# Performance work log

Hardware: AMD Instinct MI355X
Metric: run time of the kernel (lower is better)

The kernel has to match this reference:

```python
import jax, jax.numpy as jnp
import numpy as np

# Model dims (from dispatcher config)
V, H, L, I, KD = 32000, 1024, 3, 4096, 256
NH, NKV, HD = 16, 4, 64          # head_dim = H/NH = KD/NKV = 64
G = NH // NKV                     # heads per KV group = 4
B, S = 2, 1024
BLOCK, NSUB = 512, 5              # process_output: first 5 subblocks of 512 rows
TOPL = 3                          # 'deep' focus -> top-3 layers


def setup_inputs() -> dict:
    key = jax.random.key(0)
    ks = jax.random.split(key, 16)
    w = lambda k, shape: jax.random.normal(k, shape, jnp.float32) * 0.02
    return {
        "input_ids": jax.random.randint(ks[0], (B, S), 0, V),
        "emb": w(ks[1], (V, H)),              # embedding_layer
        "shortcut_emb": w(ks[2], (1000, H)),  # shortcut_embed
        "Wq": w(ks[3], (L, H, H)),            # per-layer q_proj blocks (single block0 each)
        "Wk": w(ks[4], (L, KD, H)),
        "Wv": w(ks[5], (L, KD, H)),
        "Wo": w(ks[6], (L, H, H)),
        "Wgate": w(ks[7], (L, I, H)),
        "Wup": w(ks[8], (L, I, H)),
        "Wdown": w(ks[9], (L, H, I)),
        "Wls": w(ks[10], (L, H)),             # layer_scorer
        "bls": jnp.zeros((L,), jnp.float32),
        "Wbs": w(ks[11], (1, H)),             # block_scorer
        "bbs": jnp.zeros((1,), jnp.float32),
        "Wout": w(ks[12], (4096, H)),         # output weight block (split into 512-row subblocks)
    }


def _forward(input_ids, emb, shortcut_emb, Wq, Wk, Wv, Wo,
             Wgate, Wup, Wdown, Wls, bls, Wbs, bbs, Wout):
    b, s = input_ids.shape
    # is_common: all ids < 1000 -> shortcut embedding (prev_context None on fresh call)
    is_common = jnp.all(input_ids < 1000)
    h = jnp.where(is_common,
                  shortcut_emb[jnp.clip(input_ids, 0, 999)],
                  emb[input_ids])                       # [B,S,H]

    # select_layers ('deep' focus): top-3 layers by layer_scorer on batch elem 0
    layer_scores = h.mean(axis=1)[0] @ Wls.T + bls      # [L]
    _, sel = jax.lax.top_k(layer_scores, TOPL)

    for i in range(TOPL):
        li = sel[i]                                     # dynamic layer gather
        wq, wk, wv, wo = Wq[li], Wk[li], Wv[li], Wo[li]
        wg, wu, wd = Wgate[li], Wup[li], Wdown[li]

        # scan_layer: quick q projection -> block_scorer sigmoid gate
        quick_q = h @ wq.T                              # [B,S,H]
        gate = jax.nn.sigmoid(quick_q.mean(axis=1) @ Wbs.T + bbs) > 0.5  # [B,1]

        # process_attention: manual GQA with threshold-masked softmax
        q = (h @ wq.T).reshape(b, s, NKV, G, HD).transpose(0, 2, 3, 1, 4)  # [B,KV,G,S,D]
        k = (h @ wk.T).reshape(b, s, NKV, HD).transpose(0, 2, 1, 3)        # [B,KV,S,D]
        v = (h @ wv.T).reshape(b, s, NKV, HD).transpose(0, 2, 1, 3)        # [B,KV,S,D]
        scores = jnp.einsum('bhgsd,bhqd->bhgsq', q, k) / (HD ** 0.5)       # [B,KV,G,S,S]
        aw = jax.nn.softmax(scores, axis=-1)
        aw = aw * (aw > 0.01)                           # hard threshold mask
        v_exp = jnp.broadcast_to(v[:, :, None], (b, NKV, G, s, HD))
        # NOTE: faithful to source einsum 'bhgsq,bhgsd->bhgsd': sums aw over q and scales v
        attn = jnp.einsum('bhgsq,bhgsd->bhgsd', aw, v_exp)
        attn = attn.transpose(0, 3, 1, 2, 4).reshape(b, s, H)
        attn = attn @ wo.T

        # process_mlp: gate*up (no activation in source), then down
        new_h = ((attn @ wg.T) * (attn @ wu.T)) @ wd.T

        h = jnp.where(gate[:, :, None], new_h, h)       # scan_layer gate per batch elem

    # process_output: concat first 5 subblocks of 512 rows, matmul with transpose
    combined = Wout[:BLOCK * NSUB]                      # [2560, H]
    return h @ combined.T                               # [B,S,2560]


def reference(input_ids, emb, shortcut_emb, Wq, Wk, Wv, Wo,
              Wgate, Wup, Wdown, Wls, bls, Wbs, bbs, Wout):
    return _forward(input_ids, emb, shortcut_emb, Wq, Wk, Wv, Wo,
                    Wgate, Wup, Wdown, Wls, bls, Wbs, bbs, Wout)
```

## Files before the change

kernel.cpp:

```cpp
#include <hip/hip_runtime.h>
#include <hip/hip_bf16.h>

constexpr int kH = 1024, kS = 1024, kNH = 16, kI = 4096, kNOUT = 2560;
constexpr int kQKVN = 1536;

typedef __attribute__((ext_vector_type(8))) short short8v;
typedef __attribute__((ext_vector_type(4))) float f32x4;
typedef unsigned short u16;

#define MFMA16 __builtin_amdgcn_mfma_f32_16x16x32_bf16

__device__ __forceinline__ u16 f2bf(float f) {
  unsigned u = __float_as_uint(f);
  return (u16)((u + 0x7fffu + ((u >> 16) & 1u)) >> 16);
}
__device__ __forceinline__ float bf2f(u16 u) {
  return __uint_as_float(((unsigned)u) << 16);
}
__device__ __forceinline__ unsigned cvt2bf(float lo, float hi) {
  unsigned r;
  asm("v_cvt_pk_bf16_f32 %0, %1, %2" : "=v"(r) : "v"(lo), "v"(hi));
  return r;
}
__device__ __forceinline__ void gload16(void* lds, const void* g) {
  __builtin_amdgcn_global_load_lds(
      (const __attribute__((address_space(1))) unsigned int*)g,
      (__attribute__((address_space(3))) unsigned int*)lds, 16, 0, 0);
}

constexpr long OFF_H    = 0;
constexpr long OFF_HMP  = OFF_H + 2097152;
constexpr long OFF_INT  = OFF_HMP + 16384;
constexpr long OFF_GV   = OFF_INT + 64;
constexpr long OFF_HBF  = OFF_GV + 3072;
constexpr long OFF_QKV  = OFF_HBF + 1048576;
constexpr long OFF_ATT  = OFF_QKV + 1572864;
constexpr long OFF_OBF  = OFF_ATT + 1048576;
constexpr long OFF_PBF  = OFF_OBF + 1048576;

__global__ void embed_gv_kernel(const int* __restrict__ ids, const float* __restrict__ emb,
                                const float* __restrict__ semb, const float* __restrict__ Wq,
                                const float* __restrict__ Wbs, float* __restrict__ h,
                                u16* __restrict__ hbf, float* __restrict__ gv,
                                int* __restrict__ ip) {
  int bid = blockIdx.x, tid = threadIdx.x;
  if (bid < 2048) {
    __shared__ int oks;
    if (tid == 0) oks = 1;
    __syncthreads();
    int ok = 1;
    for (int i = tid; i < 2048; i += 256) ok &= (ids[i] < 1000) ? 1 : 0;
    if (!ok) atomicAnd(&oks, 0);
    __syncthreads();
    int common = oks;
    long row = bid;
    int id = ids[row];
    int cid = id < 0 ? 0 : (id > 999 ? 999 : id);
    const float4* s4 = (const float4*)(common ? semb + (long)cid * kH : emb + (long)id * kH);
    float4 v = s4[tid];
    *((float4*)(h + row * kH) + tid) = v;
    ushort4 u;
    u.x = f2bf(v.x); u.y = f2bf(v.y); u.z = f2bf(v.z); u.w = f2bf(v.w);
    *((ushort4*)(hbf + row * kH) + tid) = u;
  } else if (bid < 2240) {
    int q = bid - 2048;
    int l = q >> 6, j0 = (q & 63) * 16;
    int jj = tid & 15, cg = tid >> 4;
    const float* wq = Wq + (long)l * 1048576;
    float acc = 0.f;
    for (int c = cg * 64; c < cg * 64 + 64; ++c)
      acc += Wbs[c] * wq[(long)c * kH + j0 + jj];
    __shared__ float red[256];
    red[tid] = acc;
    __syncthreads();
    if (tid < 16) {
      float s = 0.f;
      #pragma unroll
      for (int g = 0; g < 16; ++g) s += red[g * 16 + tid];
      gv[l * 1024 + j0 + tid] = s;
    }
  } else {
    if (tid < 32) ip[tid] = 0;
  }
}

template <int FIRST>
__global__ __launch_bounds__(256) void hmean_fused_kernel(
    const float* __restrict__ h, float* __restrict__ hmp, const float* __restrict__ gv,
    const float* __restrict__ Wls, const float* __restrict__ bls,
    const float* __restrict__ bbs, int* __restrict__ ip, int layer_i,
    int* __restrict__ cnt) {
  int tid = threadIdx.x;
  int c = blockIdx.x * 256 + tid, b = blockIdx.y, z = blockIdx.z;
  float a = 0.f;
  if (!ip[16 + b]) {
    const float* p = h + ((long)b << 20) + ((long)z << 17) + c;
    #pragma unroll 4
    for (int r = 0; r < 128; ++r) a += p[(long)r << 10];
  }
  hmp[z * 2048 + b * 1024 + c] = a;
  __threadfence();
  __syncthreads();
  __shared__ int lastf;
  if (tid == 0) lastf = (atomicAdd(cnt, 1) == 63) ? 1 : 0;
  __syncthreads();
  if (!lastf) return;
  __threadfence();

  float hm0[4], hm1[4];
  #pragma unroll
  for (int u = 0; u < 4; ++u) {
    int j = tid + u * 256;
    float s0 = 0.f, s1 = 0.f;
    #pragma unroll
    for (int z2 = 0; z2 < 8; ++z2) {
      s0 += hmp[z2 * 2048 + j];
      s1 += hmp[z2 * 2048 + 1024 + j];
    }
    hm0[u] = s0; hm1[u] = s1;
  }
  __shared__ float red[3][256];
  __shared__ int sli;
  int li;
  if constexpr (FIRST) {
    float a0 = 0.f, a1 = 0.f, a2 = 0.f;
    #pragma unroll
    for (int u = 0; u < 4; ++u) {
      int j = tid + u * 256;
      a0 += hm0[u] * Wls[j];
      a1 += hm0[u] * Wls[kH + j];
      a2 += hm0[u] * Wls[2 * kH + j];
    }
    red[0][tid] = a0; red[1][tid] = a1; red[2][tid] = a2;
    __syncthreads();
    for (int st = 128; st; st >>= 1) {
      if (tid < st) {
        red[0][tid] += red[0][tid + st];
        red[1][tid] += red[1][tid + st];
        red[2][tid] += red[2][tid + st];
      }
      __syncthreads();
    }
    if (tid == 0) {
      float sc[3] = {red[0][0] * (1.f / kS) + bls[0], red[1][0] * (1.f / kS) + bls[1],
                     red[2][0] * (1.f / kS) + bls[2]};
      int aa = 0;
      if (sc[1] > sc[aa]) aa = 1;
      if (sc[2] > sc[aa]) aa = 2;
      int b2 = -1; float bb = -3.4e38f;
      for (int i = 0; i < 3; ++i)
        if (i != aa && sc[i] > bb) { bb = sc[i]; b2 = i; }
      ip[1] = aa; ip[2] = b2; ip[3] = 3 - aa - b2;
      sli = aa;
    }
    __syncthreads();
    li = sli;
  } else {
    li = ip[1 + layer_i];
  }
  float g0 = 0.f, g1 = 0.f;
  #pragma unroll
  for (int u = 0; u < 4; ++u) {
    int j = tid + u * 256;
    float v = gv[li * 1024 + j];
    g0 += v * hm0[u];
    g1 += v * hm1[u];
  }
  __syncthreads();
  red[0][tid] = g0; red[1][tid] = g1;
  __syncthreads();
  for (int st = 128; st; st >>= 1) {
    if (tid < st) { red[0][tid] += red[0][tid + st]; red[1][tid] += red[1][tid + st]; }
    __syncthreads();
  }
  if (tid == 0) {
    int* g = ip + 4 + 2 * layer_i;
    g[0] = ((red[0][0] * (1.f / kS) + bbs[0]) > 0.f) ? 1 : 0;
    g[1] = ((red[1][0] * (1.f / kS) + bbs[0]) > 0.f) ? 1 : 0;
  }
}

template <int MODE>
__global__ __launch_bounds__(256) void gemm_bf_kernel(
    const u16* __restrict__ A, const float* __restrict__ Bf0, const float* __restrict__ Bf1,
    const float* __restrict__ Bf2, void* __restrict__ C0,
    int N, int K, const int* __restrict__ li_p,
    const int* __restrict__ gate, const int* __restrict__ hz) {
  __shared__ u16 As[128 * 64];
  __shared__ u16 Bs[64 * 64];

  const int m0 = blockIdx.y * 128, n0 = blockIdx.x * 64;
  const int tid = threadIdx.x;
  const int bb = m0 >> 10;

  if (MODE == 4 && hz != nullptr && hz[bb]) {
    int r = tid >> 1, cb = n0 + (tid & 1) * 32;
    float* c0 = (float*)C0 + (long)(m0 + r) * N + cb;
    float4 z4 = make_float4(0.f, 0.f, 0.f, 0.f);
    #pragma unroll
    for (int j = 0; j < 32; j += 4) *(float4*)(c0 + j) = z4;
    return;
  }
  if (MODE == 0) {
    if (!gate[bb]) return;
    if (hz != nullptr && hz[bb]) return;
  }

  long li = (MODE == 4) ? 0 : (long)(*li_p);
  const float* bsrc;
  if constexpr (MODE == 0) {
    if (n0 < 1024)      bsrc = Bf0 + li * 1048576 + (long)n0 * kH;
    else if (n0 < 1280) bsrc = Bf1 + li * 262144 + (long)(n0 - 1024) * kH;
    else                bsrc = Bf2 + li * 262144 + (long)(n0 - 1280) * kH;
  } else {
    bsrc = Bf0 + (long)n0 * kH;
  }

  const int wave = tid >> 6, lane = tid & 63;
  const int lr = lane & 15, lg = lane >> 4;
  const int wm = wave >> 1, wn = wave & 1;

  f32x4 acc[4][2] = {};

  const int sr = tid >> 3, sc8 = tid & 7;
  const int sr1 = (tid + 256) >> 3;

  for (int k0 = 0; k0 < K; k0 += 64) {
    #pragma unroll
    for (int j = 0; j < 4; ++j) {
      int c = tid + j * 256;
      int r = c >> 3, c8 = c & 7;
      gload16((char*)As + (wave * 64 + j * 256) * 16,
              A + (long)(m0 + r) * K + k0 + ((c8 ^ (r & 7)) * 8));
    }
    #pragma unroll
    for (int j = 0; j < 2; ++j) {
      int r = j ? sr1 : sr, c8 = sc8;
      const float* p = bsrc + (long)r * K + k0 + c8 * 8;
      float4 v0 = *(const float4*)p;
      float4 v1 = *(const float4*)(p + 4);
      union { short8v s8; unsigned u[4]; } uo;
      uo.u[0] = cvt2bf(v0.x, v0.y);
      uo.u[1] = cvt2bf(v0.z, v0.w);
      uo.u[2] = cvt2bf(v1.x, v1.y);
      uo.u[3] = cvt2bf(v1.z, v1.w);
      *(short8v*)((char*)Bs + ((r * 128 + c8 * 16) ^ ((r & 7) << 4))) = uo.s8;
    }
    __syncthreads();
    #pragma unroll
    for (int kh = 0; kh < 2; ++kh) {
      const int kb = kh * 64 + lg * 16;
      short8v av[4], bv[2];
      #pragma unroll
      for (int mi = 0; mi < 4; ++mi) {
        int r = wm * 64 + mi * 16 + lr;
        av[mi] = *(const short8v*)((const char*)As + ((r * 128 + kb) ^ ((r & 7) << 4)));
      }
      #pragma unroll
      for (int ni = 0; ni < 2; ++ni) {
        int r = wn * 32 + ni * 16 + lr;
        bv[ni] = *(const short8v*)((const char*)Bs + ((r * 128 + kb) ^ ((r & 7) << 4)));
      }
      #pragma unroll
      for (int mi = 0; mi < 4; ++mi)
        #pragma unroll
        for (int ni = 0; ni < 2; ++ni)
          acc[mi][ni] = MFMA16(av[mi], bv[ni], acc[mi][ni], 0, 0, 0);
    }
    __syncthreads();
  }
  #pragma unroll
  for (int mi = 0; mi < 4; ++mi)
    #pragma unroll
    for (int ni = 0; ni < 2; ++ni)
      #pragma unroll
      for (int r = 0; r < 4; ++r) {
        long idx = (long)(m0 + wm * 64 + mi * 16 + lg * 4 + r) * N +
                   (n0 + wn * 32 + ni * 16 + lr);
        float v = acc[mi][ni][r];
        if constexpr (MODE == 0) ((u16*)C0)[idx] = f2bf(v);
        else ((float*)C0)[idx] = v;
      }
}

__device__ __forceinline__ void dev_barrier(int* cnt, int target) {
  __syncthreads();
  __threadfence();
  if (threadIdx.x == 0) {
    atomicAdd(cnt, 1);
    while (atomicAdd(cnt, 0) < target) __builtin_amdgcn_s_sleep(8);
  }
  __syncthreads();
  __threadfence();
}

template <int PH>
__device__ __forceinline__ void mlp_tile(int t, long li, const u16* __restrict__ A,
                                         const float* __restrict__ B0base,
                                         const float* __restrict__ B1base,
                                         void* __restrict__ C0, void* __restrict__ C1,
                                         int ac0, int ac1, u16* As, u16* Bs, u16* Bs1) {
  constexpr bool USE_B1 = (PH == 1);
  constexpr int N = (PH == 1) ? 4096 : 1024;
  constexpr int K = (PH == 2) ? 4096 : 1024;
  const int tid = threadIdx.x;
  const int tm = t & 15, tn = t >> 4;
  const int m0 = tm * 128, n0 = tn * 64;
  if (!((tm >> 3) ? ac1 : ac0)) return;

  const float* bsrc;
  const float* bsrc1 = nullptr;
  if constexpr (PH == 0) {
    bsrc = B0base + li * 1048576 + (long)n0 * 1024;
  } else if constexpr (PH == 1) {
    bsrc = B0base + li * 4194304 + (long)n0 * 1024;
    bsrc1 = B1base + li * 4194304 + (long)n0 * 1024;
  } else {
    bsrc = B0base + li * 4194304 + (long)n0 * 4096;
  }

  const int wave = tid >> 6, lane = tid & 63;
  const int lr = lane & 15, lg = lane >> 4;
  const int wm = wave >> 1, wn = wave & 1;

  f32x4 acc[4][2] = {};
  f32x4 acc1[USE_B1 ? 4 : 1][2] = {};

  const int sr = tid >> 3, sc8 = tid & 7;
  const int sr1 = (tid + 256) >> 3;

  for (int k0 = 0; k0 < K; k0 += 64) {
    #pragma unroll
    for (int j = 0; j < 4; ++j) {
      int c = tid + j * 256;
      int r = c >> 3, c8 = c & 7;
      gload16((char*)As + (wave * 64 + j * 256) * 16,
              A + (long)(m0 + r) * K + k0 + ((c8 ^ (r & 7)) * 8));
    }
    #pragma unroll
    for (int j = 0; j < 2; ++j) {
      int r = j ? sr1 : sr, c8 = sc8;
      const float* p = bsrc + (long)r * K + k0 + c8 * 8;
      float4 v0 = *(const float4*)p;
      float4 v1 = *(const float4*)(p + 4);
      union { short8v s8; unsigned u[4]; } uo;
      uo.u[0] = cvt2bf(v0.x, v0.y);
      uo.u[1] = cvt2bf(v0.z, v0.w);
      uo.u[2] = cvt2bf(v1.x, v1.y);
      uo.u[3] = cvt2bf(v1.z, v1.w);
      *(short8v*)((char*)Bs + ((r * 128 + c8 * 16) ^ ((r & 7) << 4))) = uo.s8;
      if constexpr (USE_B1) {
        const float* p1 = bsrc1 + (long)r * K + k0 + c8 * 8;
        float4 w0 = *(const float4*)p1;
        float4 w1 = *(const float4*)(p1 + 4);
        union { short8v s8; unsigned u[4]; } uo1;
        uo1.u[0] = cvt2bf(w0.x, w0.y);
        uo1.u[1] = cvt2bf(w0.z, w0.w);
        uo1.u[2] = cvt2bf(w1.x, w1.y);
        uo1.u[3] = cvt2bf(w1.z, w1.w);
        *(short8v*)((char*)Bs1 + ((r * 128 + c8 * 16) ^ ((r & 7) << 4))) = uo1.s8;
      }
    }
    __syncthreads();
    #pragma unroll
    for (int kh = 0; kh < 2; ++kh) {
      const int kb = kh * 64 + lg * 16;
      short8v av[4], bv[2], b1v[2];
      #pragma unroll
      for (int mi = 0; mi < 4; ++mi) {
        int r = wm * 64 + mi * 16 + lr;
        av[mi] = *(const short8v*)((const char*)As + ((r * 128 + kb) ^ ((r & 7) << 4)));
      }
      #pragma unroll
      for (int ni = 0; ni < 2; ++ni) {
        int r = wn * 32 + ni * 16 + lr;
        int byte = (r * 128 + kb) ^ ((r & 7) << 4);
        bv[ni] = *(const short8v*)((const char*)Bs + byte);
        if constexpr (USE_B1) b1v[ni] = *(const short8v*)((const char*)Bs1 + byte);
      }
      #pragma unroll
      for (int mi = 0; mi < 4; ++mi)
        #pragma unroll
        for (int ni = 0; ni < 2; ++ni) {
          acc[mi][ni] = MFMA16(av[mi], bv[ni], acc[mi][ni], 0, 0, 0);
          if constexpr (USE_B1)
            acc1[mi][ni] = MFMA16(av[mi], b1v[ni], acc1[mi][ni], 0, 0, 0);
        }
    }
    __syncthreads();
  }
  #pragma unroll
  for (int mi = 0; mi < 4; ++mi)
    #pragma unroll
    for (int ni = 0; ni < 2; ++ni)
      #pragma unroll
      for (int r = 0; r < 4; ++r) {
        long idx = (long)(m0 + wm * 64 + mi * 16 + lg * 4 + r) * N +
                   (n0 + wn * 32 + ni * 16 + lr);
        float v = acc[mi][ni][r];
        if constexpr (PH == 0) ((u16*)C0)[idx] = f2bf(v);
        if constexpr (PH == 1) ((u16*)C0)[idx] = f2bf(v * acc1[mi][ni][r]);
        if constexpr (PH == 2) { ((float*)C0)[idx] = v; ((u16*)C1)[idx] = f2bf(v); }
      }
}

__global__ __launch_bounds__(256) void mlp_kernel(
    const u16* __restrict__ ATT, const float* __restrict__ Wo, const float* __restrict__ Wg,
    const float* __restrict__ Wu, const float* __restrict__ Wd, u16* __restrict__ Obf,
    u16* __restrict__ Pbf, float* __restrict__ h, u16* __restrict__ hbf,
    const int* __restrict__ li_p, const int* __restrict__ gate,
    const int* __restrict__ act, int* __restrict__ hzwr, int* __restrict__ cnt2) {
  const int tid = threadIdx.x, bid = blockIdx.x;
  int g0 = gate[0], g1 = gate[1];
  int a0 = act[0], a1 = act[1];
  if (bid == 0 && tid == 0) {
    if (g0) hzwr[0] = a0 ? 0 : 1;
    if (g1) hzwr[1] = a1 ? 0 : 1;
  }
  int ac0 = g0 && a0, ac1 = g1 && a1;
  if (!ac0 && !ac1) return;

  __shared__ u16 As[128 * 64];
  __shared__ u16 Bs[64 * 64];
  __shared__ u16 Bs1[64 * 64];
  long li = (long)(*li_p);

  mlp_tile<0>(bid, li, ATT, Wo, nullptr, Obf, nullptr, ac0, ac1, As, Bs, Bs1);
  dev_barrier(cnt2 + 0, 256);
  for (int t = bid; t < 1024; t += 256)
    mlp_tile<1>(t, li, Obf, Wg, Wu, Pbf, nullptr, ac0, ac1, As, Bs, Bs1);
  dev_barrier(cnt2 + 1, 256);
  mlp_tile<2>(bid, li, Pbf, Wd, nullptr, h, hbf, ac0, ac1, As, Bs, Bs1);
}

__global__ __launch_bounds__(256) void rowsum_kernel(
    const u16* __restrict__ QKV, const int* __restrict__ gate, int* __restrict__ act,
    const int* __restrict__ hz, u16* __restrict__ ATT) {
  int b = blockIdx.z;
  if (!gate[b] || hz[b]) return;
  int kvg = blockIdx.y, qt = blockIdx.x;
  int tid = threadIdx.x;
  int w = tid >> 6, lane = tid & 63, lr = lane & 15, lg = lane >> 4;

  __shared__ float sm[4][64], ss[4][64], st[4][64], srs[64];
  __shared__ int sflags;
  if (tid == 0) sflags = 0;

  long qrow = ((long)b << 10) + qt * 16 + lr;
  short8v qlo[4], qhi[4];
  #pragma unroll
  for (int hh = 0; hh < 4; ++hh) {
    const u16* qp = QKV + qrow * kQKVN + (kvg * 4 + hh) * 64 + lg * 8;
    qlo[hh] = *(const short8v*)qp;
    qhi[hh] = *(const short8v*)(qp + 32);
  }
  const u16* kb0 = QKV + (((long)b << 10) + w * 256 + lr) * kQKVN + 1024 + kvg * 64 + lg * 8;

  float s[4][4], pm[4][4];
  #pragma unroll
  for (int hh = 0; hh < 4; ++hh)
    #pragma unroll
    for (int i = 0; i < 4; ++i) { s[hh][i] = 0.f; pm[hh][i] = -3e38f; }
  for (int kt = 0; kt < 16; ++kt) {
    const u16* kp = kb0 + (long)kt * 16 * kQKVN;
    short8v klo = *(const short8v*)kp;
    short8v khi = *(const short8v*)(kp + 32);
    #pragma unroll
    for (int hh = 0; hh < 4; ++hh) {
      f32x4 c = {0.f, 0.f, 0.f, 0.f};
      c = MFMA16(qlo[hh], klo, c, 0, 0, 0);
      c = MFMA16(qhi[hh], khi, c, 0, 0, 0);
      #pragma unroll
      for (int i = 0; i < 4; ++i) {
        float x = c[i] * 0.125f;
        s[hh][i] += __expf(x);
        pm[hh][i] = fmaxf(pm[hh][i], x);
      }
    }
  }
  #pragma unroll
  for (int off = 1; off < 16; off <<= 1)
    #pragma unroll
    for (int hh = 0; hh < 4; ++hh)
      #pragma unroll
      for (int i = 0; i < 4; ++i) {
        s[hh][i] += __shfl_xor(s[hh][i], off);
        pm[hh][i] = fmaxf(pm[hh][i], __shfl_xor(pm[hh][i], off));
      }
  if (lr == 0)
    #pragma unroll
    for (int hh = 0; hh < 4; ++hh)
      #pragma unroll
      for (int i = 0; i < 4; ++i) {
        sm[w][hh * 16 + lg * 4 + i] = pm[hh][i];
        ss[w][hh * 16 + lg * 4 + i] = s[hh][i];
      }
  __syncthreads();
  float Mg[4][4], Sg[4][4];
  int myfl = 0;
  #pragma unroll
  for (int hh = 0; hh < 4; ++hh)
    #pragma unroll
    for (int i = 0; i < 4; ++i) {
      int q = hh * 16 + lg * 4 + i;
      float mm = fmaxf(fmaxf(sm[0][q], sm[1][q]), fmaxf(sm[2][q], sm[3][q]));
      float SS = ss[0][q] + ss[1][q] + ss[2][q] + ss[3][q];
      Mg[hh][i] = mm; Sg[hh][i] = SS;
      if (mm > 60.f) myfl |= 2;
      if (__expf(mm) > 0.01f * SS) myfl |= 1;
    }
  if (myfl) atomicOr(&sflags, myfl);
  __syncthreads();
  int flags = sflags;

  if (flags & 2) {
    #pragma unroll
    for (int hh = 0; hh < 4; ++hh)
      #pragma unroll
      for (int i = 0; i < 4; ++i) s[hh][i] = 0.f;
    for (int kt = 0; kt < 16; ++kt) {
      const u16* kp = kb0 + (long)kt * 16 * kQKVN;
      short8v klo = *(const short8v*)kp;
      short8v khi = *(const short8v*)(kp + 32);
      #pragma unroll
      for (int hh = 0; hh < 4; ++hh) {
        f32x4 c = {0.f, 0.f, 0.f, 0.f};
        c = MFMA16(qlo[hh], klo, c, 0, 0, 0);
        c = MFMA16(qhi[hh], khi, c, 0, 0, 0);
        #pragma unroll
        for (int i = 0; i < 4; ++i) s[hh][i] += __expf(c[i] * 0.125f - Mg[hh][i]);
      }
    }
    #pragma unroll
    for (int off = 1; off < 16; off <<= 1)
      #pragma unroll
      for (int hh = 0; hh < 4; ++hh)
        #pragma unroll
        for (int i = 0; i < 4; ++i) s[hh][i] += __shfl_xor(s[hh][i], off);
    if (lr == 0)
      #pragma unroll
      for (int hh = 0; hh < 4; ++hh)
        #pragma unroll
        for (int i = 0; i < 4; ++i) ss[w][hh * 16 + lg * 4 + i] = s[hh][i];
    __syncthreads();
    #pragma unroll
    for (int hh = 0; hh < 4; ++hh)
      #pragma unroll
      for (int i = 0; i < 4; ++i) {
        int q = hh * 16 + lg * 4 + i;
        Sg[hh][i] = ss[0][q] + ss[1][q] + ss[2][q] + ss[3][q];
      }
    __syncthreads();
  }
  float shift = (flags & 2) ? 1.f : 0.f;

  if (flags & 1) {
    float tt[4][4] = {};
    for (int kt = 0; kt < 16; ++kt) {
      const u16* kp = kb0 + (long)kt * 16 * kQKVN;
      short8v klo = *(const short8v*)kp;
      short8v khi = *(const short8v*)(kp + 32);
      #pragma unroll
      for (int hh = 0; hh < 4; ++hh) {
        f32x4 c = {0.f, 0.f, 0.f, 0.f};
        c = MFMA16(qlo[hh], klo, c, 0, 0, 0);
        c = MFMA16(qhi[hh], khi, c, 0, 0, 0);
        #pragma unroll
        for (int i = 0; i < 4; ++i) {
          float e = __expf(c[i] * 0.125f - shift * Mg[hh][i]);
          if (e > 0.01f * Sg[hh][i]) tt[hh][i] += e;
        }
      }
    }
    #pragma unroll
    for (int off = 1; off < 16; off <<= 1)
      #pragma unroll
      for (int hh = 0; hh < 4; ++hh)
        #pragma unroll
        for (int i = 0; i < 4; ++i) tt[hh][i] += __shfl_xor(tt[hh][i], off);
    if (lr == 0)
      #pragma unroll
      for (int hh = 0; hh < 4; ++hh)
        #pragma unroll
        for (int i = 0; i < 4; ++i) st[w][hh * 16 + lg * 4 + i] = tt[hh][i];
  }
  __syncthreads();
  if (tid < 64) {
    int hh = tid >> 4, q = tid & 15;
    int qq = hh * 16 + q;
    float T = (flags & 1) ? (st[0][qq] + st[1][qq] + st[2][qq] + st[3][qq]) : 0.f;
    float SS = ss[0][qq] + ss[1][qq] + ss[2][qq] + ss[3][qq];
    srs[qq] = T / SS;
    if (T > 0.f) atomicOr(act + b, 1);
  }
  __syncthreads();
  int hh = tid >> 6, rr = (tid >> 2) & 15, d0 = (tid & 3) * 16;
  float rv = srs[hh * 16 + rr];
  long row = ((long)b << 10) + qt * 16 + rr;
  const u16* vp = QKV + row * kQKVN + 1280 + kvg * 64 + d0;
  u16* op = ATT + row * kH + (kvg * 4 + hh) * 64 + d0;
  #pragma unroll
  for (int j = 0; j < 16; j += 4) {
    ushort4 v = *(const ushort4*)(vp + j);
    ushort4 o;
    o.x = f2bf(rv * bf2f(v.x)); o.y = f2bf(rv * bf2f(v.y));
    o.z = f2bf(rv * bf2f(v.z)); o.w = f2bf(rv * bf2f(v.w));
    *(ushort4*)(op + j) = o;
  }
}

extern "C" void kernel_launch(void* const* d_in, const int* in_sizes, int n_in,
                              void* d_out, int out_size, void* d_ws, size_t ws_size,
                              hipStream_t stream) {
  (void)in_sizes; (void)n_in; (void)out_size; (void)ws_size;
  const int*   ids  = (const int*)d_in[0];
  const float* emb  = (const float*)d_in[1];
  const float* semb = (const float*)d_in[2];
  const float* Wq   = (const float*)d_in[3];
  const float* Wk   = (const float*)d_in[4];
  const float* Wv   = (const float*)d_in[5];
  const float* Wo   = (const float*)d_in[6];
  const float* Wg   = (const float*)d_in[7];
  const float* Wu   = (const float*)d_in[8];
  const float* Wd   = (const float*)d_in[9];
  const float* Wls  = (const float*)d_in[10];
  const float* bls  = (const float*)d_in[11];
  const float* Wbs  = (const float*)d_in[12];
  const float* bbs  = (const float*)d_in[13];
  const float* Wout = (const float*)d_in[14];
  float* out = (float*)d_out;
  float* ws  = (float*)d_ws;

  float* h   = ws + OFF_H;
  float* hmp = ws + OFF_HMP;
  int* ip    = (int*)(ws + OFF_INT);
  int* sel   = ip + 1;
  int* gate  = ip + 4;
  int* act   = ip + 10;
  int* hzb   = ip + 16;
  int* cnt   = ip + 20;
  int* bar   = ip + 24;
  float* gv  = ws + OFF_GV;
  u16* hbf   = (u16*)(ws + OFF_HBF);
  u16* QKV   = (u16*)(ws + OFF_QKV);
  u16* ATT   = (u16*)(ws + OFF_ATT);
  u16* Obf   = (u16*)(ws + OFF_OBF);
  u16* Pbf   = (u16*)(ws + OFF_PBF);

  embed_gv_kernel<<<2241, 256, 0, stream>>>(ids, emb, semb, Wq, Wbs, h, hbf, gv, ip);

  for (int i = 0; i < 3; i++) {
    const int* li = sel + i;
    int* g_i = gate + 2 * i;
    int* a_i = act + 2 * i;

    if (i == 0)
      hmean_fused_kernel<1><<<dim3(4, 2, 8), 256, 0, stream>>>(h, hmp, gv, Wls, bls, bbs,
                                                               ip, 0, cnt + 0);
    else
      hmean_fused_kernel<0><<<dim3(4, 2, 8), 256, 0, stream>>>(h, hmp, gv, Wls, bls, bbs,
                                                               ip, i, cnt + i);
    gemm_bf_kernel<0><<<dim3(kQKVN / 64, 16), 256, 0, stream>>>(
        hbf, Wq, Wk, Wv, QKV, kQKVN, kH, li, g_i, hzb);
    rowsum_kernel<<<dim3(64, 4, 2), 256, 0, stream>>>(QKV, g_i, a_i, hzb, ATT);
    mlp_kernel<<<256, 256, 0, stream>>>(ATT, Wo, Wg, Wu, Wd, Obf, Pbf, h, hbf,
                                        li, g_i, a_i, hzb, bar + 2 * i);
  }
  gemm_bf_kernel<4><<<dim3(kNOUT / 64, 16), 256, 0, stream>>>(
      hbf, Wout, nullptr, nullptr, out, kNOUT, kH, nullptr, nullptr, hzb);
}
```

Before: 137.3 us.

## Fuse per-layer kernels into one persistent kernel with device-wide barriers

Replaces the four kernel launches per layer (hmean, QKV gemm, rowsum, mlp) and the final output gemm with one persistent 384-block kernel per layer. Phases are separated by a software grid barrier, and the output projection is folded into the last layer's kernel. The aim is to remove launch gaps and idle tails between the small dependent stages. In exchange it adds spin-wait barriers and requires all 384 blocks to be co-resident (launch bounds 2 per CU), or the kernel deadlocks. The barrier counters live in the ip area, which the embed kernel now zeroes more of.

```diff
diff --git a/kernel.cpp b/kernel.cpp
--- a/kernel.cpp
+++ b/kernel.cpp
@@ -3,6 +3,7 @@
 
 constexpr int kH = 1024, kS = 1024, kNH = 16, kI = 4096, kNOUT = 2560;
 constexpr int kQKVN = 1536;
+constexpr int GRID = 384;
 
 typedef __attribute__((ext_vector_type(8))) short short8v;
 typedef __attribute__((ext_vector_type(4))) float f32x4;
@@ -26,6 +27,17 @@
   __builtin_amdgcn_global_load_lds(
       (const __attribute__((address_space(1))) unsigned int*)g,
       (__attribute__((address_space(3))) unsigned int*)lds, 16, 0, 0);
+}
+
+__device__ __forceinline__ void dev_barrier(int* cnt, int target) {
+  __syncthreads();
+  __threadfence();
+  if (threadIdx.x == 0) {
+    atomicAdd(cnt, 1);
+    while (atomicAdd(cnt, 0) < target) __builtin_amdgcn_s_sleep(8);
+  }
+  __syncthreads();
+  __threadfence();
 }
 
 constexpr long OFF_H    = 0;
@@ -80,163 +92,44 @@
       gv[l * 1024 + j0 + tid] = s;
     }
   } else {
-    if (tid < 32) ip[tid] = 0;
-  }
-}
-
-template <int FIRST>
-__global__ __launch_bounds__(256) void hmean_fused_kernel(
-    const float* __restrict__ h, float* __restrict__ hmp, const float* __restrict__ gv,
-    const float* __restrict__ Wls, const float* __restrict__ bls,
-    const float* __restrict__ bbs, int* __restrict__ ip, int layer_i,
-    int* __restrict__ cnt) {
-  int tid = threadIdx.x;
-  int c = blockIdx.x * 256 + tid, b = blockIdx.y, z = blockIdx.z;
-  float a = 0.f;
-  if (!ip[16 + b]) {
-    const float* p = h + ((long)b << 20) + ((long)z << 17) + c;
-    #pragma unroll 4
-    for (int r = 0; r < 128; ++r) a += p[(long)r << 10];
-  }
-  hmp[z * 2048 + b * 1024 + c] = a;
-  __threadfence();
-  __syncthreads();
-  __shared__ int lastf;
-  if (tid == 0) lastf = (atomicAdd(cnt, 1) == 63) ? 1 : 0;
-  __syncthreads();
-  if (!lastf) return;
-  __threadfence();
-
-  float hm0[4], hm1[4];
-  #pragma unroll
-  for (int u = 0; u < 4; ++u) {
-    int j = tid + u * 256;
-    float s0 = 0.f, s1 = 0.f;
-    #pragma unroll
-    for (int z2 = 0; z2 < 8; ++z2) {
-      s0 += hmp[z2 * 2048 + j];
-      s1 += hmp[z2 * 2048 + 1024 + j];
-    }
-    hm0[u] = s0; hm1[u] = s1;
-  }
-  __shared__ float red[3][256];
-  __shared__ int sli;
-  int li;
-  if constexpr (FIRST) {
-    float a0 = 0.f, a1 = 0.f, a2 = 0.f;
-    #pragma unroll
-    for (int u = 0; u < 4; ++u) {
-      int j = tid + u * 256;
-      a0 += hm0[u] * Wls[j];
-      a1 += hm0[u] * Wls[kH + j];
-      a2 += hm0[u] * Wls[2 * kH + j];
-    }
-    red[0][tid] = a0; red[1][tid] = a1; red[2][tid] = a2;
-    __syncthreads();
-    for (int st = 128; st; st >>= 1) {
-      if (tid < st) {
-        red[0][tid] += red[0][tid + st];
-        red[1][tid] += red[1][tid + st];
-        red[2][tid] += red[2][tid + st];
-      }
-      __syncthreads();
-    }
-    if (tid == 0) {
-      float sc[3] = {red[0][0] * (1.f / kS) + bls[0], red[1][0] * (1.f / kS) + bls[1],
-                     red[2][0] * (1.f / kS) + bls[2]};
-      int aa = 0;
-      if (sc[1] > sc[aa]) aa = 1;
-      if (sc[2] > sc[aa]) aa = 2;
-      int b2 = -1; float bb = -3.4e38f;
-      for (int i = 0; i < 3; ++i)
-        if (i != aa && sc[i] > bb) { bb = sc[i]; b2 = i; }
-      ip[1] = aa; ip[2] = b2; ip[3] = 3 - aa - b2;
-      sli = aa;
-    }
-    __syncthreads();
-    li = sli;
-  } else {
-    li = ip[1 + layer_i];
-  }
-  float g0 = 0.f, g1 = 0.f;
-  #pragma unroll
-  for (int u = 0; u < 4; ++u) {
-    int j = tid + u * 256;
-    float v = gv[li * 1024 + j];
-    g0 += v * hm0[u];
-    g1 += v * hm1[u];
-  }
-  __syncthreads();
-  red[0][tid] = g0; red[1][tid] = g1;
-  __syncthreads();
-  for (int st = 128; st; st >>= 1) {
-    if (tid < st) { red[0][tid] += red[0][tid + st]; red[1][tid] += red[1][tid + st]; }
-    __syncthreads();
-  }
-  if (tid == 0) {
-    int* g = ip + 4 + 2 * layer_i;
-    g[0] = ((red[0][0] * (1.f / kS) + bbs[0]) > 0.f) ? 1 : 0;
-    g[1] = ((red[1][0] * (1.f / kS) + bbs[0]) > 0.f) ? 1 : 0;
-  }
-}
-
-template <int MODE>
-__global__ __launch_bounds__(256) void gemm_bf_kernel(
-    const u16* __restrict__ A, const float* __restrict__ Bf0, const float* __restrict__ Bf1,
-    const float* __restrict__ Bf2, void* __restrict__ C0,
-    int N, int K, const int* __restrict__ li_p,
-    const int* __restrict__ gate, const int* __restrict__ hz) {
-  __shared__ u16 As[128 * 64];
-  __shared__ u16 Bs[64 * 64];
-
-  const int m0 = blockIdx.y * 128, n0 = blockIdx.x * 64;
+    if (tid < 64) ip[tid] = 0;
+  }
+}
+
+__device__ __forceinline__ void qkv_tile(
+    int t, long li, const u16* __restrict__ A, const float* __restrict__ Wq,
+    const float* __restrict__ Wk, const float* __restrict__ Wv, u16* __restrict__ C0,
+    int g0, int g1, int hz0, int hz1, u16* As, u16* Bs) {
   const int tid = threadIdx.x;
-  const int bb = m0 >> 10;
-
-  if (MODE == 4 && hz != nullptr && hz[bb]) {
-    int r = tid >> 1, cb = n0 + (tid & 1) * 32;
-    float* c0 = (float*)C0 + (long)(m0 + r) * N + cb;
-    float4 z4 = make_float4(0.f, 0.f, 0.f, 0.f);
-    #pragma unroll
-    for (int j = 0; j < 32; j += 4) *(float4*)(c0 + j) = z4;
-    return;
-  }
-  if (MODE == 0) {
-    if (!gate[bb]) return;
-    if (hz != nullptr && hz[bb]) return;
-  }
-
-  long li = (MODE == 4) ? 0 : (long)(*li_p);
+  const int tm = t & 15, tn = t >> 4;
+  const int m0 = tm * 128, n0 = tn * 64;
+  const int hb = tm >> 3;
+  if (!(hb ? g1 : g0) || (hb ? hz1 : hz0)) return;
+
   const float* bsrc;
-  if constexpr (MODE == 0) {
-    if (n0 < 1024)      bsrc = Bf0 + li * 1048576 + (long)n0 * kH;
-    else if (n0 < 1280) bsrc = Bf1 + li * 262144 + (long)(n0 - 1024) * kH;
-    else                bsrc = Bf2 + li * 262144 + (long)(n0 - 1280) * kH;
-  } else {
-    bsrc = Bf0 + (long)n0 * kH;
-  }
+  if (n0 < 1024)      bsrc = Wq + li * 1048576 + (long)n0 * 1024;
+  else if (n0 < 1280) bsrc = Wk + li * 262144 + (long)(n0 - 1024) * 1024;
+  else                bsrc = Wv + li * 262144 + (long)(n0 - 1280) * 1024;
 
   const int wave = tid >> 6, lane = tid & 63;
   const int lr = lane & 15, lg = lane >> 4;
   const int wm = wave >> 1, wn = wave & 1;
-
   f32x4 acc[4][2] = {};
-
   const int sr = tid >> 3, sc8 = tid & 7;
   const int sr1 = (tid + 256) >> 3;
 
-  for (int k0 = 0; k0 < K; k0 += 64) {
+  for (int k0 = 0; k0 < 1024; k0 += 64) {
     #pragma unroll
     for (int j = 0; j < 4; ++j) {
       int c = tid + j * 256;
       int r = c >> 3, c8 = c & 7;
       gload16((char*)As + (wave * 64 + j * 256) * 16,
-              A + (long)(m0 + r) * K + k0 + ((c8 ^ (r & 7)) * 8));
+              A + (long)(m0 + r) * 1024 + k0 + ((c8 ^ (r & 7)) * 8));
     }
     #pragma unroll
     for (int j = 0; j < 2; ++j) {
       int r = j ? sr1 : sr, c8 = sc8;
-      const float* p = bsrc + (long)r * K + k0 + c8 * 8;
+      const float* p = bsrc + (long)r * 1024 + k0 + c8 * 8;
       float4 v0 = *(const float4*)p;
       float4 v1 = *(const float4*)(p + 4);
       union { short8v s8; unsigned u[4]; } uo;
@@ -275,23 +168,88 @@
     for (int ni = 0; ni < 2; ++ni)
       #pragma unroll
       for (int r = 0; r < 4; ++r) {
-        long idx = (long)(m0 + wm * 64 + mi * 16 + lg * 4 + r) * N +
+        long idx = (long)(m0 + wm * 64 + mi * 16 + lg * 4 + r) * kQKVN +
                    (n0 + wn * 32 + ni * 16 + lr);
-        float v = acc[mi][ni][r];
-        if constexpr (MODE == 0) ((u16*)C0)[idx] = f2bf(v);
-        else ((float*)C0)[idx] = v;
-      }
-}
-
-__device__ __forceinline__ void dev_barrier(int* cnt, int target) {
-  __syncthreads();
-  __threadfence();
-  if (threadIdx.x == 0) {
-    atomicAdd(cnt, 1);
-    while (atomicAdd(cnt, 0) < target) __builtin_amdgcn_s_sleep(8);
-  }
-  __syncthreads();
-  __threadfence();
+        C0[idx] = f2bf(acc[mi][ni][r]);
+      }
+}
+
+__device__ __forceinline__ void final_tile(int t, const u16* __restrict__ A,
+                                           const float* __restrict__ Wout,
+                                           float* __restrict__ out, int hz0, int hz1,
+                                           u16* As, u16* Bs) {
+  const int tid = threadIdx.x;
+  const int tm = t & 15, tn = t >> 4;
+  const int m0 = tm * 128, n0 = tn * 64;
+  if ((tm >> 3) ? hz1 : hz0) {
+    int r = tid >> 1, cb = n0 + (tid & 1) * 32;
+    float* c0 = out + (long)(m0 + r) * kNOUT + cb;
+    float4 z4 = make_float4(0.f, 0.f, 0.f, 0.f);
+    #pragma unroll
+    for (int j = 0; j < 32; j += 4) *(float4*)(c0 + j) = z4;
+    return;
+  }
+  const float* bsrc = Wout + (long)n0 * 1024;
+  const int wave = tid >> 6, lane = tid & 63;
+  const int lr = lane & 15, lg = lane >> 4;
+  const int wm = wave >> 1, wn = wave & 1;
+  f32x4 acc[4][2] = {};
+  const int sr = tid >> 3, sc8 = tid & 7;
+  const int sr1 = (tid + 256) >> 3;
+  for (int k0 = 0; k0 < 1024; k0 += 64) {
+    #pragma unroll
+    for (int j = 0; j < 4; ++j) {
+      int c = tid + j * 256;
+      int r = c >> 3, c8 = c & 7;
+      gload16((char*)As + (wave * 64 + j * 256) * 16,
+              A + (long)(m0 + r) * 1024 + k0 + ((c8 ^ (r & 7)) * 8));
+    }
+    #pragma unroll
+    for (int j = 0; j < 2; ++j) {
+      int r = j ? sr1 : sr, c8 = sc8;
+      const float* p = bsrc + (long)r * 1024 + k0 + c8 * 8;
+      float4 v0 = *(const float4*)p;
+      float4 v1 = *(const float4*)(p + 4);
+      union { short8v s8; unsigned u[4]; } uo;
+      uo.u[0] = cvt2bf(v0.x, v0.y);
+      uo.u[1] = cvt2bf(v0.z, v0.w);
+      uo.u[2] = cvt2bf(v1.x, v1.y);
+      uo.u[3] = cvt2bf(v1.z, v1.w);
+      *(short8v*)((char*)Bs + ((r * 128 + c8 * 16) ^ ((r & 7) << 4))) = uo.s8;
+    }
+    __syncthreads();
+    #pragma unroll
+    for (int kh = 0; kh < 2; ++kh) {
+      const int kb = kh * 64 + lg * 16;
+      short8v av[4], bv[2];
+      #pragma unroll
+      for (int mi = 0; mi < 4; ++mi) {
+        int r = wm * 64 + mi * 16 + lr;
+        av[mi] = *(const short8v*)((const char*)As + ((r * 128 + kb) ^ ((r & 7) << 4)));
+      }
+      #pragma unroll
+      for (int ni = 0; ni < 2; ++ni) {
+        int r = wn * 32 + ni * 16 + lr;
+        bv[ni] = *(const short8v*)((const char*)Bs + ((r * 128 + kb) ^ ((r & 7) << 4)));
+      }
+      #pragma unroll
+      for (int mi = 0; mi < 4; ++mi)
+        #pragma unroll
+        for (int ni = 0; ni < 2; ++ni)
+          acc[mi][ni] = MFMA16(av[mi], bv[ni], acc[mi][ni], 0, 0, 0);
+    }
+    __syncthreads();
+  }
+  #pragma unroll
+  for (int mi = 0; mi < 4; ++mi)
+    #pragma unroll
+    for (int ni = 0; ni < 2; ++ni)
+      #pragma unroll
+      for (int r = 0; r < 4; ++r) {
+        long idx = (long)(m0 + wm * 64 + mi * 16 + lg * 4 + r) * kNOUT +
+                   (n0 + wn * 32 + ni * 16 + lr);
+        out[idx] = acc[mi][ni][r];
+      }
 }
 
 template <int PH>
@@ -322,10 +280,8 @@
   const int wave = tid >> 6, lane = tid & 63;
   const int lr = lane & 15, lg = lane >> 4;
   const int wm = wave >> 1, wn = wave & 1;
-
   f32x4 acc[4][2] = {};
   f32x4 acc1[USE_B1 ? 4 : 1][2] = {};
-
   const int sr = tid >> 3, sc8 = tid & 7;
   const int sr1 = (tid + 256) >> 3;
 
@@ -404,47 +360,17 @@
       }
 }
 
-__global__ __launch_bounds__(256) void mlp_kernel(
-    const u16* __restrict__ ATT, const float* __restrict__ Wo, const float* __restrict__ Wg,
-    const float* __restrict__ Wu, const float* __restrict__ Wd, u16* __restrict__ Obf,
-    u16* __restrict__ Pbf, float* __restrict__ h, u16* __restrict__ hbf,
-    const int* __restrict__ li_p, const int* __restrict__ gate,
-    const int* __restrict__ act, int* __restrict__ hzwr, int* __restrict__ cnt2) {
-  const int tid = threadIdx.x, bid = blockIdx.x;
-  int g0 = gate[0], g1 = gate[1];
-  int a0 = act[0], a1 = act[1];
-  if (bid == 0 && tid == 0) {
-    if (g0) hzwr[0] = a0 ? 0 : 1;
-    if (g1) hzwr[1] = a1 ? 0 : 1;
-  }
-  int ac0 = g0 && a0, ac1 = g1 && a1;
-  if (!ac0 && !ac1) return;
-
-  __shared__ u16 As[128 * 64];
-  __shared__ u16 Bs[64 * 64];
-  __shared__ u16 Bs1[64 * 64];
-  long li = (long)(*li_p);
-
-  mlp_tile<0>(bid, li, ATT, Wo, nullptr, Obf, nullptr, ac0, ac1, As, Bs, Bs1);
-  dev_barrier(cnt2 + 0, 256);
-  for (int t = bid; t < 1024; t += 256)
-    mlp_tile<1>(t, li, Obf, Wg, Wu, Pbf, nullptr, ac0, ac1, As, Bs, Bs1);
-  dev_barrier(cnt2 + 1, 256);
-  mlp_tile<2>(bid, li, Pbf, Wd, nullptr, h, hbf, ac0, ac1, As, Bs, Bs1);
-}
-
-__global__ __launch_bounds__(256) void rowsum_kernel(
-    const u16* __restrict__ QKV, const int* __restrict__ gate, int* __restrict__ act,
-    const int* __restrict__ hz, u16* __restrict__ ATT) {
-  int b = blockIdx.z;
-  if (!gate[b] || hz[b]) return;
-  int kvg = blockIdx.y, qt = blockIdx.x;
+__device__ __forceinline__ void rowsum_tile(
+    int t, const u16* __restrict__ QKV, int* __restrict__ act, u16* __restrict__ ATT,
+    int g0, int g1, int hz0, int hz1,
+    float* sm_, float* ss_, float* st_, float* srs_, int* sflags_) {
+  int b = t >> 8, kvg = (t >> 6) & 3, qt = t & 63;
+  if (!(b ? g1 : g0) || (b ? hz1 : hz0)) return;
   int tid = threadIdx.x;
   int w = tid >> 6, lane = tid & 63, lr = lane & 15, lg = lane >> 4;
 
-  __shared__ float sm[4][64], ss[4][64], st[4][64], srs[64];
-  __shared__ int sflags;
-  if (tid == 0) sflags = 0;
+  __syncthreads();
+  if (tid == 0) *sflags_ = 0;
 
   long qrow = ((long)b << 10) + qt * 16 + lr;
   short8v qlo[4], qhi[4];
@@ -492,8 +418,8 @@
     for (int hh = 0; hh < 4; ++hh)
       #pragma unroll
       for (int i = 0; i < 4; ++i) {
-        sm[w][hh * 16 + lg * 4 + i] = pm[hh][i];
-        ss[w][hh * 16 + lg * 4 + i] = s[hh][i];
+        sm_[w * 64 + hh * 16 + lg * 4 + i] = pm[hh][i];
+        ss_[w * 64 + hh * 16 + lg * 4 + i] = s[hh][i];
       }
   __syncthreads();
   float Mg[4][4], Sg[4][4];
@@ -503,15 +429,15 @@
     #pragma unroll
     for (int i = 0; i < 4; ++i) {
       int q = hh * 16 + lg * 4 + i;
-      float mm = fmaxf(fmaxf(sm[0][q], sm[1][q]), fmaxf(sm[2][q], sm[3][q]));
-      float SS = ss[0][q] + ss[1][q] + ss[2][q] + ss[3][q];
+      float mm = fmaxf(fmaxf(sm_[q], sm_[64 + q]), fmaxf(sm_[128 + q], sm_[192 + q]));
+      float SS = ss_[q] + ss_[64 + q] + ss_[128 + q] + ss_[192 + q];
       Mg[hh][i] = mm; Sg[hh][i] = SS;
       if (mm > 60.f) myfl |= 2;
       if (__expf(mm) > 0.01f * SS) myfl |= 1;
     }
-  if (myfl) atomicOr(&sflags, myfl);
+  if (myfl) atomicOr(sflags_, myfl);
   __syncthreads();
-  int flags = sflags;
+  int flags = *sflags_;
 
   if (flags & 2) {
     #pragma unroll
@@ -541,14 +467,14 @@
       #pragma unroll
       for (int hh = 0; hh < 4; ++hh)
         #pragma unroll
-        for (int i = 0; i < 4; ++i) ss[w][hh * 16 + lg * 4 + i] = s[hh][i];
+        for (int i = 0; i < 4; ++i) ss_[w * 64 + hh * 16 + lg * 4 + i] = s[hh][i];
     __syncthreads();
     #pragma unroll
     for (int hh = 0; hh < 4; ++hh)
       #pragma unroll
       for (int i = 0; i < 4; ++i) {
         int q = hh * 16 + lg * 4 + i;
-        Sg[hh][i] = ss[0][q] + ss[1][q] + ss[2][q] + ss[3][q];
+        Sg[hh][i] = ss_[q] + ss_[64 + q] + ss_[128 + q] + ss_[192 + q];
       }
     __syncthreads();
   }
@@ -582,20 +508,19 @@
       #pragma unroll
       for (int hh = 0; hh < 4; ++hh)
         #pragma unroll
-        for (int i = 0; i < 4; ++i) st[w][hh * 16 + lg * 4 + i] = tt[hh][i];
+        for (int i = 0; i < 4; ++i) st_[w * 64 + hh * 16 + lg * 4 + i] = tt[hh][i];
   }
   __syncthreads();
   if (tid < 64) {
-    int hh = tid >> 4, q = tid & 15;
-    int qq = hh * 16 + q;
-    float T = (flags & 1) ? (st[0][qq] + st[1][qq] + st[2][qq] + st[3][qq]) : 0.f;
-    float SS = ss[0][qq] + ss[1][qq] + ss[2][qq] + ss[3][qq];
-    srs[qq] = T / SS;
+    int qq = tid;
+    float T = (flags & 1) ? (st_[qq] + st_[64 + qq] + st_[128 + qq] + st_[192 + qq]) : 0.f;
+    float SS = ss_[qq] + ss_[64 + qq] + ss_[128 + qq] + ss_[192 + qq];
+    srs_[qq] = T / SS;
     if (T > 0.f) atomicOr(act + b, 1);
   }
   __syncthreads();
   int hh = tid >> 6, rr = (tid >> 2) & 15, d0 = (tid & 3) * 16;
-  float rv = srs[hh * 16 + rr];
+  float rv = srs_[hh * 16 + rr];
   long row = ((long)b << 10) + qt * 16 + rr;
   const u16* vp = QKV + row * kQKVN + 1280 + kvg * 64 + d0;
   u16* op = ATT + row * kH + (kvg * 4 + hh) * 64 + d0;
@@ -606,6 +531,157 @@
     o.x = f2bf(rv * bf2f(v.x)); o.y = f2bf(rv * bf2f(v.y));
     o.z = f2bf(rv * bf2f(v.z)); o.w = f2bf(rv * bf2f(v.w));
     *(ushort4*)(op + j) = o;
+  }
+}
+
+template <int FIRST, int LAST>
+__global__ __launch_bounds__(256, 2) void layer_kernel(
+    float* __restrict__ h, float* __restrict__ hmp, const float* __restrict__ gv,
+    const float* __restrict__ Wls, const float* __restrict__ bls,
+    const float* __restrict__ bbs, int* __restrict__ ip, int layer_i,
+    u16* __restrict__ hbf,
+    const float* __restrict__ Wq, const float* __restrict__ Wk,
+    const float* __restrict__ Wv, const float* __restrict__ Wo,
+    const float* __restrict__ Wg, const float* __restrict__ Wu,
+    const float* __restrict__ Wd,
+    u16* __restrict__ QKV, u16* __restrict__ ATT, u16* __restrict__ Obf,
+    u16* __restrict__ Pbf, const float* __restrict__ Wout, float* __restrict__ out) {
+  int* cb = ip + 24 + layer_i * 8;
+  const int tid = threadIdx.x, bid = blockIdx.x;
+  __shared__ __align__(16) char smem[32768];
+  u16* As = (u16*)smem;
+  u16* Bs = (u16*)(smem + 16384);
+  u16* Bs1 = (u16*)(smem + 24576);
+  float* rsm = (float*)smem;
+  float* rss = (float*)(smem + 1024);
+  float* rst = (float*)(smem + 2048);
+  float* rsr = (float*)(smem + 3072);
+  __shared__ int sflags;
+
+  if (bid < 64) {
+    int c = (bid & 3) * 256 + tid, b = (bid >> 2) & 1, z = bid >> 3;
+    float a = 0.f;
+    if (!ip[16 + b]) {
+      const float* p = h + ((long)b << 20) + ((long)z << 17) + c;
+      #pragma unroll 4
+      for (int r = 0; r < 128; ++r) a += p[(long)r << 10];
+    }
+    hmp[z * 2048 + b * 1024 + c] = a;
+    __threadfence();
+    __syncthreads();
+    __shared__ int lastf;
+    if (tid == 0) lastf = (atomicAdd(cb + 0, 1) == 63) ? 1 : 0;
+    __syncthreads();
+    if (lastf) {
+      __threadfence();
+      float hm0[4], hm1[4];
+      #pragma unroll
+      for (int u = 0; u < 4; ++u) {
+        int j = tid + u * 256;
+        float s0 = 0.f, s1 = 0.f;
+        #pragma unroll
+        for (int z2 = 0; z2 < 8; ++z2) {
+          s0 += hmp[z2 * 2048 + j];
+          s1 += hmp[z2 * 2048 + 1024 + j];
+        }
+        hm0[u] = s0; hm1[u] = s1;
+      }
+      float (*red)[256] = (float(*)[256])smem;
+      __shared__ int sli;
+      int li;
+      if constexpr (FIRST) {
+        float a0 = 0.f, a1 = 0.f, a2 = 0.f;
+        #pragma unroll
+        for (int u = 0; u < 4; ++u) {
+          int j = tid + u * 256;
+          a0 += hm0[u] * Wls[j];
+          a1 += hm0[u] * Wls[kH + j];
+          a2 += hm0[u] * Wls[2 * kH + j];
+        }
+        red[0][tid] = a0; red[1][tid] = a1; red[2][tid] = a2;
+        __syncthreads();
+        for (int st = 128; st; st >>= 1) {
+          if (tid < st) {
+            red[0][tid] += red[0][tid + st];
+            red[1][tid] += red[1][tid + st];
+            red[2][tid] += red[2][tid + st];
+          }
+          __syncthreads();
+        }
+        if (tid == 0) {
+          float sc[3] = {red[0][0] * (1.f / kS) + bls[0], red[1][0] * (1.f / kS) + bls[1],
+                         red[2][0] * (1.f / kS) + bls[2]};
+          int aa = 0;
+          if (sc[1] > sc[aa]) aa = 1;
+          if (sc[2] > sc[aa]) aa = 2;
+          int b2 = -1; float bb = -3.4e38f;
+          for (int i = 0; i < 3; ++i)
+            if (i != aa && sc[i] > bb) { bb = sc[i]; b2 = i; }
+          ip[1] = aa; ip[2] = b2; ip[3] = 3 - aa - b2;
+          sli = aa;
+        }
+        __syncthreads();
+        li = sli;
+      } else {
+        li = ip[1 + layer_i];
+      }
+      float g0 = 0.f, g1 = 0.f;
+      #pragma unroll
+      for (int u = 0; u < 4; ++u) {
+        int j = tid + u * 256;
+        float v = gv[li * 1024 + j];
+        g0 += v * hm0[u];
+        g1 += v * hm1[u];
+      }
+      __syncthreads();
+      red[0][tid] = g0; red[1][tid] = g1;
+      __syncthreads();
+      for (int st = 128; st; st >>= 1) {
+        if (tid < st) { red[0][tid] += red[0][tid + st]; red[1][tid] += red[1][tid + st]; }
+        __syncthreads();
+      }
+      if (tid == 0) {
+        int* g = ip + 4 + 2 * layer_i;
+        g[0] = ((red[0][0] * (1.f / kS) + bbs[0]) > 0.f) ? 1 : 0;
+        g[1] = ((red[1][0] * (1.f / kS) + bbs[0]) > 0.f) ? 1 : 0;
+      }
+      __syncthreads();
+    }
+  }
+  dev_barrier(cb + 1, GRID);
+
+  long li = (long)ip[1 + layer_i];
+  int g0 = ip[4 + 2 * layer_i], g1 = ip[5 + 2 * layer_i];
+  int hz0 = ip[16], hz1 = ip[17];
+  if (g0 || g1) {
+    qkv_tile(bid, li, hbf, Wq, Wk, Wv, QKV, g0, g1, hz0, hz1, As, Bs);
+    dev_barrier(cb + 2, GRID);
+    for (int t = bid; t < 512; t += GRID)
+      rowsum_tile(t, QKV, ip + 10 + 2 * layer_i, ATT, g0, g1, hz0, hz1,
+                  rsm, rss, rst, rsr, &sflags);
+    dev_barrier(cb + 3, GRID);
+    int a0 = ip[10 + 2 * layer_i], a1 = ip[11 + 2 * layer_i];
+    int ac0 = g0 && a0, ac1 = g1 && a1;
+    int ranD = (ac0 || ac1);
+    if (ranD) {
+      if (bid < 256) mlp_tile<0>(bid, li, ATT, Wo, nullptr, Obf, nullptr, ac0, ac1, As, Bs, Bs1);
+      dev_barrier(cb + 4, GRID);
+      for (int t = bid; t < 1024; t += GRID)
+        mlp_tile<1>(t, li, Obf, Wg, Wu, Pbf, nullptr, ac0, ac1, As, Bs, Bs1);
+      dev_barrier(cb + 5, GRID);
+      if (bid < 256) mlp_tile<2>(bid, li, Pbf, Wd, nullptr, h, hbf, ac0, ac1, As, Bs, Bs1);
+    }
+    if (!LAST && bid == 0 && tid == 0) {
+      if (g0) ip[16] = a0 ? 0 : 1;
+      if (g1) ip[17] = a1 ? 0 : 1;
+    }
+    hz0 = g0 ? (a0 ? 0 : 1) : hz0;
+    hz1 = g1 ? (a1 ? 0 : 1) : hz1;
+    if (LAST && ranD) dev_barrier(cb + 6, GRID);
+  }
+  if constexpr (LAST) {
+    for (int t = bid; t < 640; t += GRID)
+      final_tile(t, hbf, Wout, out, hz0, hz1, As, Bs);
   }
 }
 
@@ -634,12 +710,6 @@
   float* h   = ws + OFF_H;
   float* hmp = ws + OFF_HMP;
   int* ip    = (int*)(ws + OFF_INT);
-  int* sel   = ip + 1;
-  int* gate  = ip + 4;
-  int* act   = ip + 10;
-  int* hzb   = ip + 16;
-  int* cnt   = ip + 20;
-  int* bar   = ip + 24;
   float* gv  = ws + OFF_GV;
   u16* hbf   = (u16*)(ws + OFF_HBF);
   u16* QKV   = (u16*)(ws + OFF_QKV);
@@ -648,24 +718,13 @@
   u16* Pbf   = (u16*)(ws + OFF_PBF);
 
   embed_gv_kernel<<<2241, 256, 0, stream>>>(ids, emb, semb, Wq, Wbs, h, hbf, gv, ip);
-
-  for (int i = 0; i < 3; i++) {
-    const int* li = sel + i;
-    int* g_i = gate + 2 * i;
-    int* a_i = act + 2 * i;
-
-    if (i == 0)
-      hmean_fused_kernel<1><<<dim3(4, 2, 8), 256, 0, stream>>>(h, hmp, gv, Wls, bls, bbs,
-                                                               ip, 0, cnt + 0);
-    else
-      hmean_fused_kernel<0><<<dim3(4, 2, 8), 256, 0, stream>>>(h, hmp, gv, Wls, bls, bbs,
-                                                               ip, i, cnt + i);
-    gemm_bf_kernel<0><<<dim3(kQKVN / 64, 16), 256, 0, stream>>>(
-        hbf, Wq, Wk, Wv, QKV, kQKVN, kH, li, g_i, hzb);
-    rowsum_kernel<<<dim3(64, 4, 2), 256, 0, stream>>>(QKV, g_i, a_i, hzb, ATT);
-    mlp_kernel<<<256, 256, 0, stream>>>(ATT, Wo, Wg, Wu, Wd, Obf, Pbf, h, hbf,
-                                        li, g_i, a_i, hzb, bar + 2 * i);
-  }
-  gemm_bf_kernel<4><<<dim3(kNOUT / 64, 16), 256, 0, stream>>>(
-      hbf, Wout, nullptr, nullptr, out, kNOUT, kH, nullptr, nullptr, hzb);
-}
+  layer_kernel<1, 0><<<GRID, 256, 0, stream>>>(h, hmp, gv, Wls, bls, bbs, ip, 0, hbf,
+                                               Wq, Wk, Wv, Wo, Wg, Wu, Wd,
+                                               QKV, ATT, Obf, Pbf, Wout, out);
+  layer_kernel<0, 0><<<GRID, 256, 0, stream>>>(h, hmp, gv, Wls, bls, bbs, ip, 1, hbf,
+                                               Wq, Wk, Wv, Wo, Wg, Wu, Wd,
+                                               QKV, ATT, Obf, Pbf, Wout, out);
+  layer_kernel<0, 1><<<GRID, 256, 0, stream>>>(h, hmp, gv, Wls, bls, bbs, ip, 2, hbf,
+                                               Wq, Wk, Wv, Wo, Wg, Wu, Wd,
+                                               QKV, ATT, Obf, Pbf, Wout, out);
+}
```

After: 535.2 us. +289.7%, slower.
